# Kernel tuning notes

Measured on AMD Instinct MI355X. Metric: run time of the kernel, lower is better.

The kernel has to match this reference:

```python
import jax, jax.numpy as jnp
import numpy as np

N_NODES = 100000
N_EDGES = 1600000
DIM = 128
N_GRAPHS = 64
N_LAYERS = 7
LEAKY_SLOPE = 0.01
BN_EPS = 1e-5


def setup_inputs() -> dict:
    key = jax.random.key(0)
    ks = jax.random.split(key, 6)
    x = jax.random.normal(ks[0], (N_NODES, DIM), dtype=jnp.float32)
    edge_index = jax.random.randint(ks[1], (2, N_EDGES), 0, N_NODES, dtype=jnp.int64)
    batch = jnp.sort(jax.random.randint(ks[2], (N_NODES,), 0, N_GRAPHS, dtype=jnp.int64))
    # GCNConv weights (Glorot-ish scale), biases, BatchNorm affine params
    Ws = jax.random.normal(ks[3], (N_LAYERS, DIM, DIM), dtype=jnp.float32) * (1.0 / np.sqrt(DIM))
    bs = jnp.zeros((N_LAYERS, DIM), dtype=jnp.float32)
    gammas = jnp.ones((N_LAYERS, DIM), dtype=jnp.float32)
    betas = jnp.zeros((N_LAYERS, DIM), dtype=jnp.float32)
    return {"x": x, "edge_index": edge_index, "batch": batch,
            "Ws": Ws, "bs": bs, "gammas": gammas, "betas": betas}


def reference(x, edge_index, batch, Ws, bs, gammas, betas):
    N = x.shape[0]
    # Add self-loops once (shared by all 7 GCNConv layers)
    loops = jnp.arange(N, dtype=edge_index.dtype)
    src = jnp.concatenate([edge_index[0], loops])  # [E+N]
    dst = jnp.concatenate([edge_index[1], loops])  # [E+N]
    # Symmetric normalization: deg over destination (incl. self-loops)
    deg = jax.ops.segment_sum(jnp.ones_like(dst, dtype=x.dtype), dst, num_segments=N)
    dinv = jax.lax.rsqrt(jnp.maximum(deg, 1.0))  # deg >= 1 from self-loops
    norm = dinv[src] * dinv[dst]                 # [E+N]

    def block(h, W, b, gamma, beta):
        # GCNConv: linear -> gather -> normalized scatter-add
        h = h @ W + b                                            # [N, D]
        msgs = h[src] * norm[:, None]                            # [E+N, D]
        h = jax.ops.segment_sum(msgs, dst, num_segments=N)       # [N, D]
        # LeakyReLU then BatchNorm (batch statistics over nodes)
        h = jax.nn.leaky_relu(h, negative_slope=LEAKY_SLOPE)
        mu = jnp.mean(h, axis=0)
        var = jnp.mean((h - mu) ** 2, axis=0)
        h = (h - mu) * jax.lax.rsqrt(var + BN_EPS) * gamma + beta
        return h

    h = x
    for i in range(N_LAYERS):
        h = block(h, Ws[i], bs[i], gammas[i], betas[i])

    # global_mean_pool over graph ids
    sums = jax.ops.segment_sum(h, batch, num_segments=N_GRAPHS)          # [G, D]
    cnt = jax.ops.segment_sum(jnp.ones((N,), h.dtype), batch, num_segments=N_GRAPHS)
    return sums / jnp.maximum(cnt, 1.0)[:, None]
```

## Files before the change

kernel.cpp:

```cpp
#include <hip/hip_runtime.h>
#include <hip/hip_fp16.h>

#define DIMM 128
#define LEAKY_S 0.01f
#define EPS_BN 1e-5f

typedef _Float16 half8 __attribute__((ext_vector_type(8)));
typedef float f32x4 __attribute__((ext_vector_type(4)));


__global__ __launch_bounds__(256) void k_deg(const int* __restrict__ dst, int* __restrict__ deg, int E, int N) {
    int i = blockIdx.x * 256 + threadIdx.x;
    if (i < E) {
        int d = dst[i];
        if ((unsigned)d < (unsigned)N) atomicAdd(&deg[d], 1);
    }
}

__global__ __launch_bounds__(256) void k_dinv(const int* __restrict__ deg, float* __restrict__ dinv, int N) {
    int i = blockIdx.x * 256 + threadIdx.x;
    if (i < N) dinv[i] = rsqrtf((float)(deg[i] + 1));
}

__global__ __launch_bounds__(256) void k_scanA(const int* __restrict__ deg, int* __restrict__ bsum, int n) {
    __shared__ int ws[4];
    int tid = threadIdx.x, lane = tid & 63, wid = tid >> 6;
    int base = blockIdx.x * 1024;
    int s = 0;
    #pragma unroll
    for (int j = 0; j < 4; ++j) {
        int i = base + j * 256 + tid;
        if (i < n) s += deg[i];
    }
    #pragma unroll
    for (int off = 32; off > 0; off >>= 1) s += __shfl_down(s, (unsigned)off, 64);
    if (lane == 0) ws[wid] = s;
    __syncthreads();
    if (tid == 0) bsum[blockIdx.x] = ws[0] + ws[1] + ws[2] + ws[3];
}

__global__ __launch_bounds__(64) void k_scanB(const int* __restrict__ bsum, int* __restrict__ bofs,
                                              int* __restrict__ rowptr, int nb, int n) {
    if (threadIdx.x == 0) {
        int run = 0;
        for (int j = 0; j < nb; ++j) { bofs[j] = run; run += bsum[j]; }
        rowptr[n] = run;
    }
}

__global__ __launch_bounds__(1024) void k_scanC(const int* __restrict__ deg, const int* __restrict__ bofs,
                                                int* __restrict__ rowptr, int n) {
    __shared__ int wsum[16];
    int tid = threadIdx.x, lane = tid & 63, wid = tid >> 6;
    int i = blockIdx.x * 1024 + tid;
    int v = (i < n) ? deg[i] : 0;
    int s = v;
    #pragma unroll
    for (int off = 1; off < 64; off <<= 1) {
        int t = __shfl_up(s, (unsigned)off, 64);
        if (lane >= off) s += t;
    }
    if (lane == 63) wsum[wid] = s;
    __syncthreads();
    if (wid == 0 && lane < 16) {
        int ws = wsum[lane];
        #pragma unroll
        for (int off = 1; off < 16; off <<= 1) {
            int t = __shfl_up(ws, (unsigned)off, 64);
            if (lane >= off) ws += t;
        }
        wsum[lane] = ws;
    }
    __syncthreads();
    int woff = wid ? wsum[wid - 1] : 0;
    if (i < n) rowptr[i] = bofs[blockIdx.x] + woff + (s - v);
}

__global__ __launch_bounds__(256) void k_fill(const int* __restrict__ src, const int* __restrict__ dst,
                                              const int* __restrict__ rowptr, int* __restrict__ cursor,
                                              const float* __restrict__ dinv,
                                              int2* __restrict__ csr, int E, int N) {
    int i = blockIdx.x * 256 + threadIdx.x;
    if (i < E) {
        int d = dst[i], s = src[i];
        if ((unsigned)d < (unsigned)N && (unsigned)s < (unsigned)N) {
            int pos = atomicAdd(&cursor[d], 1);
            int idx = rowptr[d] + pos;
            csr[idx] = make_int2(s, __float_as_int(dinv[s] * dinv[d]));
        }
    }
}


__global__ __launch_bounds__(256) void k_wprep(const float* __restrict__ Ws, __half* __restrict__ Wt) {
    int l = blockIdx.y;
    int i = blockIdx.x * 256 + threadIdx.x;
    int n = i >> 7, k = i & 127;
    Wt[(size_t)l * DIMM * DIMM + n * DIMM + k] = __float2half(Ws[(size_t)l * DIMM * DIMM + k * DIMM + n]);
}


__global__ __launch_bounds__(256) void k_gemm(const void* __restrict__ A, const __half* __restrict__ Wt,
                                              const float* __restrict__ bias, const float* __restrict__ ss,
                                              __half* __restrict__ out, int N, int a_half) {
    __shared__ char smem[128 * 272];
    int tid = threadIdx.x;
    int lane = tid & 63, wid = tid >> 6;
    int quad = lane >> 4, lm = lane & 15;
    int row0 = blockIdx.x * 128;

    {
        int seg = tid & 31;
        int col = seg * 4;
        float4 sc = *(const float4*)(ss + col);
        float4 sh = *(const float4*)(ss + 128 + col);
        const float*  Af = (const float*)A;
        const __half* Ah = (const __half*)A;
        for (int i = tid; i < 128 * 32; i += 256) {
            int r = i >> 5;
            int gr = row0 + r;
            float4 v = make_float4(0.f, 0.f, 0.f, 0.f);
            if (gr < N) {
                if (a_half) {
                    union { uint2 u; __half2 h2[2]; } ld;
                    ld.u = *(const uint2*)(Ah + (size_t)gr * DIMM + col);
                    float2 f0 = __half22float2(ld.h2[0]);
                    float2 f1 = __half22float2(ld.h2[1]);
                    v = make_float4(f0.x, f0.y, f1.x, f1.y);
                } else {
                    v = *(const float4*)(Af + (size_t)gr * DIMM + col);
                }
                v.x = v.x * sc.x + sh.x; v.y = v.y * sc.y + sh.y;
                v.z = v.z * sc.z + sh.z; v.w = v.w * sc.w + sh.w;
            }
            union { _Float16 h[4]; uint2 u; } pk;
            pk.h[0] = (_Float16)v.x; pk.h[1] = (_Float16)v.y;
            pk.h[2] = (_Float16)v.z; pk.h[3] = (_Float16)v.w;
            *(uint2*)(smem + r * 272 + seg * 8) = pk.u;
        }
    }

    f32x4 acc[2][8];
    #pragma unroll
    for (int c = 0; c < 8; ++c) {
        float bc = bias[c * 16 + lm];
        acc[0][c] = (f32x4){bc, bc, bc, bc};
        acc[1][c] = acc[0][c];
    }
    __syncthreads();

    const _Float16* Wt16 = (const _Float16*)Wt;
    #pragma unroll
    for (int kc = 0; kc < 4; ++kc) {
        half8 a0 = *(const half8*)(smem + (wid * 32 + lm) * 272 + kc * 64 + quad * 16);
        half8 a1 = *(const half8*)(smem + (wid * 32 + 16 + lm) * 272 + kc * 64 + quad * 16);
        #pragma unroll
        for (int c = 0; c < 8; ++c) {
            half8 b = *(const half8*)(Wt16 + (c * 16 + lm) * DIMM + kc * 32 + quad * 8);
            acc[0][c] = __builtin_amdgcn_mfma_f32_16x16x32_f16(a0, b, acc[0][c], 0, 0, 0);
            acc[1][c] = __builtin_amdgcn_mfma_f32_16x16x32_f16(a1, b, acc[1][c], 0, 0, 0);
        }
    }

    __syncthreads();
    #pragma unroll
    for (int r = 0; r < 2; ++r)
        #pragma unroll
        for (int c = 0; c < 8; ++c)
            #pragma unroll
            for (int i = 0; i < 4; ++i) {
                int rit = wid * 32 + r * 16 + quad * 4 + i;
                int col = c * 16 + lm;
                *(_Float16*)(smem + rit * 256 + col * 2) = (_Float16)acc[r][c][i];
            }
    __syncthreads();
    for (int i = tid; i < 128 * 16; i += 256) {
        int r = i >> 4, seg = i & 15;
        int gr = row0 + r;
        if (gr < N)
            ((uint4*)(out + (size_t)gr * DIMM))[seg] = ((const uint4*)(smem + r * 256))[seg];
    }
}


__global__ __launch_bounds__(256) void k_agg(const __half* __restrict__ t, __half* __restrict__ out,
                                             const int* __restrict__ rowptr, const int2* __restrict__ csr,
                                             const float* __restrict__ dinv,
                                             float* __restrict__ stats, int N, int nwaves) {
    int tid = threadIdx.x;
    int lane = tid & 63, wid = tid >> 6;
    int grp = lane >> 4;
    int l16 = lane & 15;
    int gw = blockIdx.x * 4 + wid;

    float sx[8] = {0.f, 0.f, 0.f, 0.f, 0.f, 0.f, 0.f, 0.f};
    float qx[8] = {0.f, 0.f, 0.f, 0.f, 0.f, 0.f, 0.f, 0.f};

    for (int node = gw; node < N; node += nwaves) {
        float di = dinv[node];
        float sn = di * di;
        float v[8] = {0.f, 0.f, 0.f, 0.f, 0.f, 0.f, 0.f, 0.f};
        if (grp == 0) {
            union { half8 h; __half2 h2[4]; } u;
            u.h = *(const half8*)(t + (size_t)node * DIMM + l16 * 8);
            #pragma unroll
            for (int p = 0; p < 4; ++p) {
                float2 f = __half22float2(u.h2[p]);
                v[2 * p]     = sn * f.x;
                v[2 * p + 1] = sn * f.y;
            }
        }
        int e = rowptr[node], e1 = rowptr[node + 1];
        for (; e + 16 <= e1; e += 16) {
            #pragma unroll
            for (int j = 0; j < 4; ++j) {
                int2 cw = csr[e + 4 * j + grp];
                float wgt = __int_as_float(cw.y);
                union { half8 h; __half2 h2[4]; } u;
                u.h = *(const half8*)(t + (size_t)cw.x * DIMM + l16 * 8);
                #pragma unroll
                for (int p = 0; p < 4; ++p) {
                    float2 f = __half22float2(u.h2[p]);
                    v[2 * p]     = fmaf(wgt, f.x, v[2 * p]);
                    v[2 * p + 1] = fmaf(wgt, f.y, v[2 * p + 1]);
                }
            }
        }
        if (e < e1) {
            #pragma unroll
            for (int j = 0; j < 4; ++j) {
                int idx = e + 4 * j + grp;
                if (idx < e1) {
                    int2 cw = csr[idx];
                    float wgt = __int_as_float(cw.y);
                    union { half8 h; __half2 h2[4]; } u;
                    u.h = *(const half8*)(t + (size_t)cw.x * DIMM + l16 * 8);
                    #pragma unroll
                    for (int p = 0; p < 4; ++p) {
                        float2 f = __half22float2(u.h2[p]);
                        v[2 * p]     = fmaf(wgt, f.x, v[2 * p]);
                        v[2 * p + 1] = fmaf(wgt, f.y, v[2 * p + 1]);
                    }
                }
            }
        }
        #pragma unroll
        for (int i = 0; i < 8; ++i) {
            v[i] += __shfl_down(v[i], 32, 64);
            v[i] += __shfl_down(v[i], 16, 64);
        }
        if (grp == 0) {
            union { _Float16 h[8]; uint4 u4; } pk;
            #pragma unroll
            for (int i = 0; i < 8; ++i) {
                v[i] = v[i] > 0.f ? v[i] : LEAKY_S * v[i];
                sx[i] += v[i];
                qx[i] += v[i] * v[i];
                pk.h[i] = (_Float16)v[i];
            }
            *(uint4*)(out + (size_t)node * DIMM + l16 * 8) = pk.u4;
        }
    }

    __shared__ float red[4 * 128];
    if (grp == 0) {
        *(float4*)(red + wid * 128 + l16 * 8)     = make_float4(sx[0], sx[1], sx[2], sx[3]);
        *(float4*)(red + wid * 128 + l16 * 8 + 4) = make_float4(sx[4], sx[5], sx[6], sx[7]);
    }
    __syncthreads();
    if (tid < 128) {
        float s = red[tid] + red[128 + tid] + red[256 + tid] + red[384 + tid];
        atomicAdd(&stats[tid], s);
    }
    __syncthreads();
    if (grp == 0) {
        *(float4*)(red + wid * 128 + l16 * 8)     = make_float4(qx[0], qx[1], qx[2], qx[3]);
        *(float4*)(red + wid * 128 + l16 * 8 + 4) = make_float4(qx[4], qx[5], qx[6], qx[7]);
    }
    __syncthreads();
    if (tid < 128) {
        float s = red[tid] + red[128 + tid] + red[256 + tid] + red[384 + tid];
        atomicAdd(&stats[128 + tid], s);
    }
}

__global__ __launch_bounds__(128) void k_bnfin(const float* __restrict__ stats, const float* __restrict__ gamma,
                                               const float* __restrict__ beta, float* __restrict__ ss_out,
                                               float inv_n) {
    int c = threadIdx.x;
    float mu  = stats[c] * inv_n;
    float var = stats[128 + c] * inv_n - mu * mu;
    float a = gamma[c] * rsqrtf(var + EPS_BN);
    ss_out[c]       = a;
    ss_out[128 + c] = beta[c] - mu * a;
}

__global__ __launch_bounds__(128) void k_init_ss(float* __restrict__ ss) {
    int c = threadIdx.x;
    ss[c] = 1.0f;
    ss[128 + c] = 0.0f;
}


__global__ __launch_bounds__(64) void k_cnt_bs(const int* __restrict__ batch, int* __restrict__ cnt, int N, int G) {
    int g = blockIdx.x * 64 + threadIdx.x;
    if (g >= G) return;
    int lo = 0, hi = N;
    while (lo < hi) { int mid = (lo + hi) >> 1; if (batch[mid] < g) lo = mid + 1; else hi = mid; }
    int lb = lo;
    lo = 0; hi = N;
    while (lo < hi) { int mid = (lo + hi) >> 1; if (batch[mid] <= g) lo = mid + 1; else hi = mid; }
    cnt[g] = lo - lb;
}

__global__ __launch_bounds__(128) void k_pool(const __half* __restrict__ h, const int* __restrict__ batch,
                                              float* __restrict__ pool, int N, int G) {
    const int CHUNK = 128;
    int start = blockIdx.x * CHUNK;
    if (start >= N) return;
    int end = min(start + CHUNK, N);
    int tid = threadIdx.x;
    float acc = 0.f;
    int cur = batch[start];
    for (int n = start; n < end; ++n) {
        int g = batch[n];
        if (g != cur) {
            if ((unsigned)cur < (unsigned)G) atomicAdd(&pool[(size_t)cur * DIMM + tid], acc);
            acc = 0.f; cur = g;
        }
        acc += __half2float(h[(size_t)n * DIMM + tid]);
    }
    if ((unsigned)cur < (unsigned)G) atomicAdd(&pool[(size_t)cur * DIMM + tid], acc);
}

__global__ __launch_bounds__(256) void k_poolfin(const float* __restrict__ pool, const int* __restrict__ cnt,
                                                 const float* __restrict__ ss, float* __restrict__ out, int G) {
    int idx = blockIdx.x * 256 + threadIdx.x;
    if (idx < G * DIMM) {
        int g = idx >> 7, c = idx & 127;
        float m = pool[idx] / (float)max(cnt[g], 1);
        out[idx] = ss[c] * m + ss[128 + c];
    }
}


extern "C" void kernel_launch(void* const* d_in, const int* in_sizes, int n_in,
                              void* d_out, int out_size, void* d_ws, size_t ws_size,
                              hipStream_t stream) {
    const float* x      = (const float*)d_in[0];
    const int*   ei     = (const int*)d_in[1];
    const int*   batch  = (const int*)d_in[2];
    const float* Ws     = (const float*)d_in[3];
    const float* bs     = (const float*)d_in[4];
    const float* gammas = (const float*)d_in[5];
    const float* betas  = (const float*)d_in[6];
    float* outp = (float*)d_out;

    int N = in_sizes[2];
    int E = in_sizes[1] / 2;
    int L = in_sizes[3] / (DIMM * DIMM);
    int G = out_size / DIMM;

    const int* srcv = ei;
    const int* dstv = ei + E;

    int nb = (N + 1023) / 1024;

    char* w = (char*)d_ws;
    auto alloc = [&](size_t bytes) { char* p = w; w += (bytes + 511) & ~size_t(511); return p; };
    int*    deg    = (int*)   alloc((size_t)N * 4);
    int*    cursor = (int*)   alloc((size_t)N * 4);
    int*    rowptr = (int*)   alloc((size_t)(N + 1) * 4);
    int*    bsum   = (int*)   alloc((size_t)nb * 4);
    int*    bofs   = (int*)   alloc((size_t)nb * 4);
    int2*   csr    = (int2*)  alloc((size_t)E * 8);
    float*  dinv   = (float*) alloc((size_t)N * 4);
    __half* hA     = (__half*)alloc((size_t)N * DIMM * 2);
    __half* hB     = (__half*)alloc((size_t)N * DIMM * 2);
    __half* Wt     = (__half*)alloc((size_t)L * DIMM * DIMM * 2);
    float*  stats  = (float*) alloc((size_t)L * 256 * 4);
    float*  ss     = (float*) alloc((size_t)(L + 1) * 256 * 4);
    float*  pool   = (float*) alloc((size_t)G * DIMM * 4);
    int*    cnt    = (int*)   alloc((size_t)G * 4);

    hipMemsetAsync(deg,    0, (size_t)N * 4, stream);
    hipMemsetAsync(cursor, 0, (size_t)N * 4, stream);
    hipMemsetAsync(stats,  0, (size_t)L * 256 * 4, stream);
    hipMemsetAsync(pool,   0, (size_t)G * DIMM * 4, stream);

    k_init_ss<<<1, 128, 0, stream>>>(ss);
    k_wprep<<<dim3(64, L), 256, 0, stream>>>(Ws, Wt);
    k_deg  <<<(E + 255) / 256, 256, 0, stream>>>(dstv, deg, E, N);
    k_dinv <<<(N + 255) / 256, 256, 0, stream>>>(deg, dinv, N);
    k_scanA<<<nb, 256, 0, stream>>>(deg, bsum, N);
    k_scanB<<<1, 64, 0, stream>>>(bsum, bofs, rowptr, nb, N);
    k_scanC<<<nb, 1024, 0, stream>>>(deg, bofs, rowptr, N);
    k_fill <<<(E + 255) / 256, 256, 0, stream>>>(srcv, dstv, rowptr, cursor, dinv, csr, E, N);

    const void* cur_in = (const void*)x;
    int a_half = 0;
    for (int l = 0; l < L; ++l) {
        k_gemm<<<(N + 127) / 128, 256, 0, stream>>>(cur_in, Wt + (size_t)l * DIMM * DIMM,
                                                    bs + (size_t)l * DIMM, ss + (size_t)l * 256, hA, N, a_half);
        const int nblk = 2048;
        k_agg<<<nblk, 256, 0, stream>>>(hA, hB, rowptr, csr, dinv,
                                        stats + (size_t)l * 256, N, nblk * 4);
        k_bnfin<<<1, 128, 0, stream>>>(stats + (size_t)l * 256, gammas + (size_t)l * DIMM,
                                       betas + (size_t)l * DIMM, ss + (size_t)(l + 1) * 256, 1.0f / (float)N);
        cur_in = (const void*)hB;
        a_half = 1;
    }

    k_cnt_bs<<<(G + 63) / 64, 64, 0, stream>>>(batch, cnt, N, G);
    k_pool<<<(N + 127) / 128, 128, 0, stream>>>(hB, batch, pool, N, G);
    k_poolfin<<<(G * DIMM + 255) / 256, 256, 0, stream>>>(pool, cnt, ss + (size_t)L * 256, outp, G);
}
```

Before: 1.282 ms.

## Prefetch next node's row bounds and widen edge gather batch in aggregation

Restructures the aggregation loop so the next node's rowptr bounds and dinv are loaded one iteration ahead. Each pass now gathers 32 edges (8 per lane group) with clamped indices and zeroed weights for padding, replacing the separate full-chunk and tail loops. The self-loop feature load is issued before the edge loop, and the kernel adds a launch bound of 8 blocks per CU. The intent is to put more gathers in flight and take the rowptr load latency off the critical path. In exchange, register pressure rises and short rows do wasted padded loads.

```diff
diff --git a/kernel.cpp b/kernel.cpp
--- a/kernel.cpp
+++ b/kernel.cpp
@@ -183,10 +183,10 @@
 }
 
 
-__global__ __launch_bounds__(256) void k_agg(const __half* __restrict__ t, __half* __restrict__ out,
-                                             const int* __restrict__ rowptr, const int2* __restrict__ csr,
-                                             const float* __restrict__ dinv,
-                                             float* __restrict__ stats, int N, int nwaves) {
+__global__ __launch_bounds__(256, 8) void k_agg(const __half* __restrict__ t, __half* __restrict__ out,
+                                                const int* __restrict__ rowptr, const int2* __restrict__ csr,
+                                                const float* __restrict__ dinv,
+                                                float* __restrict__ stats, int N, int nwaves) {
     int tid = threadIdx.x;
     int lane = tid & 63, wid = tid >> 6;
     int grp = lane >> 4;
@@ -196,54 +196,54 @@
     float sx[8] = {0.f, 0.f, 0.f, 0.f, 0.f, 0.f, 0.f, 0.f};
     float qx[8] = {0.f, 0.f, 0.f, 0.f, 0.f, 0.f, 0.f, 0.f};
 
-    for (int node = gw; node < N; node += nwaves) {
-        float di = dinv[node];
-        float sn = di * di;
+    int node = gw;
+    int e0 = 0, e1 = 0;
+    float di = 0.f;
+    if (node < N) { e0 = rowptr[node]; e1 = rowptr[node + 1]; di = dinv[node]; }
+
+    while (node < N) {
+        int nxt = node + nwaves;
+        int ep0 = 0, ep1 = 0;
+        float dip = 0.f;
+        if (nxt < N) { ep0 = rowptr[nxt]; ep1 = rowptr[nxt + 1]; dip = dinv[nxt]; }
+
+        union { half8 h; __half2 h2[4]; } us;
+        us.h = *(const half8*)(t + ((size_t)(unsigned)node << 7) + l16 * 8);
+
         float v[8] = {0.f, 0.f, 0.f, 0.f, 0.f, 0.f, 0.f, 0.f};
-        if (grp == 0) {
-            union { half8 h; __half2 h2[4]; } u;
-            u.h = *(const half8*)(t + (size_t)node * DIMM + l16 * 8);
+
+        for (int e = e0; e < e1; e += 32) {
+            int2 c[8];
+            int last = e1 - 1;
             #pragma unroll
-            for (int p = 0; p < 4; ++p) {
-                float2 f = __half22float2(u.h2[p]);
-                v[2 * p]     = sn * f.x;
-                v[2 * p + 1] = sn * f.y;
+            for (int j = 0; j < 8; ++j) {
+                int idx = e + 4 * j + grp;
+                int idxc = idx < last ? idx : last;
+                c[j] = csr[idxc];
+                if (idx >= e1) c[j].y = 0;
             }
-        }
-        int e = rowptr[node], e1 = rowptr[node + 1];
-        for (; e + 16 <= e1; e += 16) {
             #pragma unroll
-            for (int j = 0; j < 4; ++j) {
-                int2 cw = csr[e + 4 * j + grp];
-                float wgt = __int_as_float(cw.y);
-                union { half8 h; __half2 h2[4]; } u;
-                u.h = *(const half8*)(t + (size_t)cw.x * DIMM + l16 * 8);
+            for (int j = 0; j < 8; ++j) {
+                float wgt = __int_as_float(c[j].y);
+                union { half8 h; __half2 h2[4]; } g;
+                g.h = *(const half8*)(t + ((size_t)(unsigned)c[j].x << 7) + l16 * 8);
                 #pragma unroll
                 for (int p = 0; p < 4; ++p) {
-                    float2 f = __half22float2(u.h2[p]);
+                    float2 f = __half22float2(g.h2[p]);
                     v[2 * p]     = fmaf(wgt, f.x, v[2 * p]);
                     v[2 * p + 1] = fmaf(wgt, f.y, v[2 * p + 1]);
                 }
             }
         }
-        if (e < e1) {
-            #pragma unroll
-            for (int j = 0; j < 4; ++j) {
-                int idx = e + 4 * j + grp;
-                if (idx < e1) {
-                    int2 cw = csr[idx];
-                    float wgt = __int_as_float(cw.y);
-                    union { half8 h; __half2 h2[4]; } u;
-                    u.h = *(const half8*)(t + (size_t)cw.x * DIMM + l16 * 8);
-                    #pragma unroll
-                    for (int p = 0; p < 4; ++p) {
-                        float2 f = __half22float2(u.h2[p]);
-                        v[2 * p]     = fmaf(wgt, f.x, v[2 * p]);
-                        v[2 * p + 1] = fmaf(wgt, f.y, v[2 * p + 1]);
-                    }
-                }
-            }
-        }
+
+        float sn = (grp == 0) ? di * di : 0.f;
+        #pragma unroll
+        for (int p = 0; p < 4; ++p) {
+            float2 f = __half22float2(us.h2[p]);
+            v[2 * p]     = fmaf(sn, f.x, v[2 * p]);
+            v[2 * p + 1] = fmaf(sn, f.y, v[2 * p + 1]);
+        }
+
         #pragma unroll
         for (int i = 0; i < 8; ++i) {
             v[i] += __shfl_down(v[i], 32, 64);
@@ -258,8 +258,10 @@
                 qx[i] += v[i] * v[i];
                 pk.h[i] = (_Float16)v[i];
             }
-            *(uint4*)(out + (size_t)node * DIMM + l16 * 8) = pk.u4;
-        }
+            *(uint4*)(out + ((size_t)(unsigned)node << 7) + l16 * 8) = pk.u4;
+        }
+
+        node = nxt; e0 = ep0; e1 = ep1; di = dip;
     }
 
     __shared__ float red[4 * 128];
```

Result: slower. 2.250 ms (+75.5%).
